# Optimization experiments

Hardware: AMD Instinct MI355X
Metric: run time of the kernel (lower is better)

The kernel has to match this reference:

```python
import jax, jax.numpy as jnp
import numpy as np

CAPACITY = 0.5


def setup_inputs() -> dict:
    key = jax.random.key(0)
    ks = jax.random.split(key, 5)
    B, L, D = 4, 4096, 1024
    Dff = 4 * D
    x = jax.random.normal(ks[0], (B, L, D), dtype=jnp.float32)
    w_router = jax.random.normal(ks[1], (D,), dtype=jnp.float32) / np.sqrt(D)
    w_bypass = jax.random.normal(ks[2], (D, D), dtype=jnp.float32) / np.sqrt(D)
    w1 = jax.random.normal(ks[3], (Dff, D), dtype=jnp.float32) / np.sqrt(D)
    w2 = jax.random.normal(ks[4], (D, Dff), dtype=jnp.float32) / np.sqrt(Dff)
    return {"x": x, "w_router": w_router, "w_bypass": w_bypass, "w1": w1, "w2": w2}


def _block_fn(x, w1, w2):
    # stand-in for the expensive full block: 2-layer GELU FFN (torch Linear: y = x W^T)
    h = jax.nn.gelu(jnp.einsum('bld,fd->blf', x, w1))
    return jnp.einsum('blf,df->bld', h, w2)


def reference(x, w_router, w_bypass, w1, w2):
    B, L, D = x.shape
    k = max(1, int(L * CAPACITY))  # static
    if k >= L:
        return _block_fn(x, w1, w2)
    # router scores (B, L)
    scores = jnp.einsum('bld,d->bl', x, w_router)
    _, top_idx = jax.lax.top_k(scores, k)          # (B, k)
    top_idx = jnp.sort(top_idx, axis=-1)           # (B, k), sorted positions
    # gather selected tokens -> (B, k, D)
    x_sel = jnp.take_along_axis(x, top_idx[:, :, None], axis=1)
    out_sel = _block_fn(x_sel, w1, w2)             # (B, k, D)
    # bypass path for all tokens
    output = jnp.einsum('bld,ed->ble', x, w_bypass)
    # scatter block outputs back onto selected positions
    b_idx = jnp.arange(B)[:, None]                 # (B, 1)
    output = output.at[b_idx, top_idx].set(out_sel)
    return output
```

## Files before the change

### kernel.cpp

```cpp
#include <hip/hip_runtime.h>
#include <stdint.h>
#include <math.h>


typedef __attribute__((ext_vector_type(8))) __bf16 bf16x8;
typedef __attribute__((ext_vector_type(4))) __bf16 bf16x4;
typedef __attribute__((ext_vector_type(4))) float f32x4;

__device__ __forceinline__ void async_cp16(const __bf16* g, __bf16* l) {
    __builtin_amdgcn_global_load_lds(
        (__attribute__((address_space(1))) void*)g,
        (__attribute__((address_space(3))) void*)l,
        16, 0, 0);
}

__device__ __forceinline__ float gelu_tanh(float x) {
    float x3 = x * x * x;
    float t = tanhf(0.7978845608028654f * (x + 0.044715f * x3));
    return 0.5f * x * (1.0f + t);
}

__global__ __launch_bounds__(256) void cvt_bf16(
    const float* __restrict__ in, __bf16* __restrict__ out, int n)
{
    int i = (blockIdx.x * blockDim.x + threadIdx.x) * 8;
    if (i >= n) return;
    float4 a = *(const float4*)(in + i);
    float4 b = *(const float4*)(in + i + 4);
    bf16x8 v;
    v[0] = (__bf16)a.x; v[1] = (__bf16)a.y; v[2] = (__bf16)a.z; v[3] = (__bf16)a.w;
    v[4] = (__bf16)b.x; v[5] = (__bf16)b.y; v[6] = (__bf16)b.z; v[7] = (__bf16)b.w;
    *(bf16x8*)(out + i) = v;
}

__global__ __launch_bounds__(256) void router_scores(
    const float* __restrict__ x, const float* __restrict__ wr,
    float* __restrict__ scores)
{
    int wid  = (blockIdx.x * blockDim.x + threadIdx.x) >> 6;
    int lane = threadIdx.x & 63;
    const float* row = x + (size_t)wid * 1024;
    double s = 0.0;
    #pragma unroll
    for (int it = 0; it < 4; ++it) {
        int base = it * 256 + lane * 4;
        float4 xv = *(const float4*)(row + base);
        float4 wv = *(const float4*)(wr + base);
        s += (double)xv.x * wv.x + (double)xv.y * wv.y
           + (double)xv.z * wv.z + (double)xv.w * wv.w;
    }
    #pragma unroll
    for (int off = 32; off > 0; off >>= 1) s += __shfl_down(s, off, 64);
    if (lane == 0) scores[wid] = (float)s;
}

__global__ __launch_bounds__(1024) void topk_build(
    const float* __restrict__ scores,
    int* __restrict__ sel_rows, int* __restrict__ byp_rows)
{
    const int L = 4096, K = 2048;
    __shared__ unsigned long long key[4096];
    __shared__ int flag[4096];
    __shared__ int tsum[1024];
    int b = blockIdx.x, t = threadIdx.x;

    for (int i = t; i < L; i += 1024) {
        unsigned u = __float_as_uint(scores[b * L + i]);
        u = (u & 0x80000000u) ? ~u : (u | 0x80000000u);
        key[i] = ((unsigned long long)u << 32) | (unsigned)(L - 1 - i);
    }
    __syncthreads();

    for (int kk = 2; kk <= L; kk <<= 1) {
        for (int j = kk >> 1; j > 0; j >>= 1) {
            for (int i = t; i < L; i += 1024) {
                int p = i ^ j;
                if (p > i) {
                    unsigned long long a = key[i], c = key[p];
                    bool sw = ((i & kk) == 0) ? (a < c) : (a > c);
                    if (sw) { key[i] = c; key[p] = a; }
                }
            }
            __syncthreads();
        }
    }

    for (int s = t; s < L; s += 1024) {
        int idx = (L - 1) - (int)(key[s] & 0xffffffffu);
        flag[idx] = (s < K) ? 1 : 0;
    }
    __syncthreads();

    int base = t * 4;
    int f0 = flag[base], f1 = flag[base+1], f2 = flag[base+2], f3 = flag[base+3];
    tsum[t] = f0 + f1 + f2 + f3;
    __syncthreads();
    for (int off = 1; off < 1024; off <<= 1) {
        int v = tsum[t];
        if (t >= off) v += tsum[t - off];
        __syncthreads();
        tsum[t] = v;
        __syncthreads();
    }
    int run = (t > 0) ? tsum[t - 1] : 0;
    int fl[4] = {f0, f1, f2, f3};
    #pragma unroll
    for (int j = 0; j < 4; ++j) {
        int idx = base + j;
        if (fl[j]) { sel_rows[b * K + run] = b * L + idx; run++; }
        else       { byp_rows[b * (L - K) + (idx - run)] = b * L + idx; }
    }
}

template <bool GATHER_A, bool SCATTER_OUT, bool GELU_ACT, typename OT>
__global__ __launch_bounds__(256) void gemm_async(
    const __bf16* __restrict__ A, const __bf16* __restrict__ W,
    OT* __restrict__ Out, const int* __restrict__ rows,
    int K, int lda, int ldo)
{
    constexpr int BM = 128, BK = 64;
    __shared__ __align__(16) __bf16 As[BM * BK];
    __shared__ __align__(16) __bf16 Bs[BM * BK];
    __shared__ int rs[BM];

    const int tid = threadIdx.x;
    const int m0 = blockIdx.y * BM, n0 = blockIdx.x * BM;
    if (tid < BM) rs[tid] = rows ? rows[m0 + tid] : (m0 + tid);
    __syncthreads();

    const int sub = tid >> 3;
    const int gc  = (tid & 7) ^ (sub & 7);
    const __bf16* aptr[4]; const __bf16* bptr[4];
    __bf16* adst[4]; __bf16* bdst[4];
    #pragma unroll
    for (int i = 0; i < 4; ++i) {
        int row = i * 32 + sub;
        int ar  = GATHER_A ? rs[row] : (m0 + row);
        aptr[i] = A + (size_t)ar * lda + gc * 8;
        bptr[i] = W + (size_t)(n0 + row) * K + gc * 8;
        adst[i] = As + (i * 256 + tid) * 8;
        bdst[i] = Bs + (i * 256 + tid) * 8;
    }

    f32x4 acc[4][4] = {};
    const int lane = tid & 63;
    const int wv = tid >> 6;
    const int wr = (wv >> 1) * 64, wc = (wv & 1) * 64;
    const int r = lane & 15, quad = lane >> 4;

    for (int k0 = 0; k0 < K; k0 += BK) {
        #pragma unroll
        for (int i = 0; i < 4; ++i) async_cp16(aptr[i] + k0, adst[i]);
        #pragma unroll
        for (int i = 0; i < 4; ++i) async_cp16(bptr[i] + k0, bdst[i]);
        __syncthreads();

        #pragma unroll
        for (int ks = 0; ks < 2; ++ks) {
            bf16x8 af[4], bfm[4];
            #pragma unroll
            for (int mi = 0; mi < 4; ++mi) {
                int row = wr + mi * 16 + r;
                int swz = (ks * 4 + quad) ^ (row & 7);
                af[mi] = *(const bf16x8*)(As + row * BK + swz * 8);
            }
            #pragma unroll
            for (int ni = 0; ni < 4; ++ni) {
                int row = wc + ni * 16 + r;
                int swz = (ks * 4 + quad) ^ (row & 7);
                bfm[ni] = *(const bf16x8*)(Bs + row * BK + swz * 8);
            }
            #pragma unroll
            for (int mi = 0; mi < 4; ++mi)
                #pragma unroll
                for (int ni = 0; ni < 4; ++ni)
                    acc[mi][ni] = __builtin_amdgcn_mfma_f32_16x16x32_bf16(
                        af[mi], bfm[ni], acc[mi][ni], 0, 0, 0);
        }
        __syncthreads();
    }

    #pragma unroll
    for (int mi = 0; mi < 4; ++mi) {
        #pragma unroll
        for (int reg = 0; reg < 4; ++reg) {
            int rowl = wr + mi * 16 + quad * 4 + reg;
            int orow = SCATTER_OUT ? rs[rowl] : (m0 + rowl);
            OT* op = Out + (size_t)orow * ldo + n0;
            #pragma unroll
            for (int ni = 0; ni < 4; ++ni) {
                float v = acc[mi][ni][reg];
                if (GELU_ACT) v = gelu_tanh(v);
                op[wc + ni * 16 + r] = (OT)v;
            }
        }
    }
}

template <typename AT, typename OT, bool GATHER_A, bool SCATTER_OUT, bool GELU_ACT>
__global__ __launch_bounds__(256) void gemm_bt(
    const AT* __restrict__ A, const float* __restrict__ W,
    OT* __restrict__ Out, const int* __restrict__ rows,
    int K, int lda, int ldo)
{
    constexpr int BM = 128, BK = 64, LDK = 72;
    __shared__ __align__(16) __bf16 As[BM * LDK];
    __shared__ __align__(16) __bf16 Bs[BM * LDK];
    __shared__ int rs[BM];

    const int tid = threadIdx.x;
    const int m0 = blockIdx.y * BM, n0 = blockIdx.x * BM;
    if (tid < BM) rs[tid] = rows ? rows[m0 + tid] : (m0 + tid);
    __syncthreads();

    constexpr bool A_F32 = (sizeof(AT) == 4);
    constexpr int A_PASS = A_F32 ? 8 : 4;
    const int a_rowg = A_F32 ? (tid >> 4) : (tid >> 3);
    const int a_col  = A_F32 ? (tid & 15) : (tid & 7);
    const AT* aptr[A_PASS];
    int a_lrow[A_PASS];
    #pragma unroll
    for (int it = 0; it < A_PASS; ++it) {
        int row = it * (A_F32 ? 16 : 32) + a_rowg;
        int ar = GATHER_A ? rs[row] : (m0 + row);
        aptr[it] = A + (size_t)ar * lda + a_col * (A_F32 ? 4 : 8);
        a_lrow[it] = row;
    }
    const int b_rowg = tid >> 4, b_col = tid & 15;
    const float* bptr[8];
    #pragma unroll
    for (int it = 0; it < 8; ++it)
        bptr[it] = W + (size_t)(n0 + it * 16 + b_rowg) * K + b_col * 4;

    f32x4 acc[4][4] = {};
    const int lane = tid & 63;
    const int wv = tid >> 6;
    const int wr = (wv >> 1) * 64, wc = (wv & 1) * 64;
    const int r = lane & 15, quad = lane >> 4;

    for (int k0 = 0; k0 < K; k0 += BK) {
        #pragma unroll
        for (int it = 0; it < A_PASS; ++it) {
            if (A_F32) {
                float4 v = *(const float4*)((const float*)aptr[it] + k0);
                bf16x4 w;
                w[0] = (__bf16)v.x; w[1] = (__bf16)v.y;
                w[2] = (__bf16)v.z; w[3] = (__bf16)v.w;
                *(bf16x4*)(As + a_lrow[it] * LDK + a_col * 4) = w;
            } else {
                bf16x8 v = *(const bf16x8*)((const __bf16*)aptr[it] + k0);
                *(bf16x8*)(As + a_lrow[it] * LDK + a_col * 8) = v;
            }
        }
        #pragma unroll
        for (int it = 0; it < 8; ++it) {
            float4 v = *(const float4*)(bptr[it] + k0);
            bf16x4 w;
            w[0] = (__bf16)v.x; w[1] = (__bf16)v.y;
            w[2] = (__bf16)v.z; w[3] = (__bf16)v.w;
            *(bf16x4*)(Bs + (it * 16 + b_rowg) * LDK + b_col * 4) = w;
        }
        __syncthreads();

        #pragma unroll
        for (int ks = 0; ks < 2; ++ks) {
            bf16x8 af[4], bfm[4];
            #pragma unroll
            for (int mi = 0; mi < 4; ++mi) {
                int row = wr + mi * 16 + r;
                af[mi] = *(const bf16x8*)(As + row * LDK + (ks * 4 + quad) * 8);
            }
            #pragma unroll
            for (int ni = 0; ni < 4; ++ni) {
                int row = wc + ni * 16 + r;
                bfm[ni] = *(const bf16x8*)(Bs + row * LDK + (ks * 4 + quad) * 8);
            }
            #pragma unroll
            for (int mi = 0; mi < 4; ++mi)
                #pragma unroll
                for (int ni = 0; ni < 4; ++ni)
                    acc[mi][ni] = __builtin_amdgcn_mfma_f32_16x16x32_bf16(
                        af[mi], bfm[ni], acc[mi][ni], 0, 0, 0);
        }
        __syncthreads();
    }

    #pragma unroll
    for (int mi = 0; mi < 4; ++mi) {
        #pragma unroll
        for (int reg = 0; reg < 4; ++reg) {
            int rowl = wr + mi * 16 + quad * 4 + reg;
            int orow = SCATTER_OUT ? rs[rowl] : (m0 + rowl);
            OT* op = Out + (size_t)orow * ldo + n0;
            #pragma unroll
            for (int ni = 0; ni < 4; ++ni) {
                float v = acc[mi][ni][reg];
                if (GELU_ACT) v = gelu_tanh(v);
                op[wc + ni * 16 + r] = (OT)v;
            }
        }
    }
}

extern "C" void kernel_launch(void* const* d_in, const int* in_sizes, int n_in,
                              void* d_out, int out_size, void* d_ws, size_t ws_size,
                              hipStream_t stream) {
    (void)in_sizes; (void)n_in; (void)out_size;
    const float* x  = (const float*)d_in[0];
    const float* wr = (const float*)d_in[1];
    const float* wb = (const float*)d_in[2];
    const float* w1 = (const float*)d_in[3];
    const float* w2 = (const float*)d_in[4];
    float* out = (float*)d_out;

    const int B = 4, L = 4096, D = 1024, DFF = 4096, KSEL = 2048;
    const int M = B * KSEL;
    const int NTOK = B * L;

    char* ws = (char*)d_ws;
    float* scores = (float*)ws;            ws += sizeof(float) * (size_t)NTOK;
    int* sel_rows = (int*)ws;              ws += sizeof(int) * (size_t)M;
    int* byp_rows = (int*)ws;              ws += sizeof(int) * (size_t)M;
    uintptr_t up = ((uintptr_t)ws + 255) & ~(uintptr_t)255;

    size_t n_x = (size_t)NTOK * D, n_wb = (size_t)D * D;
    size_t n_w1 = (size_t)DFF * D, n_w2 = (size_t)D * DFF;
    size_t n_h = (size_t)M * DFF;
    size_t needA = (up - (uintptr_t)d_ws)
                 + 2 * (n_x + n_wb + n_w1 + n_w2 + n_h) + 1024;

    router_scores<<<NTOK / 4, 256, 0, stream>>>(x, wr, scores);
    topk_build<<<B, 1024, 0, stream>>>(scores, sel_rows, byp_rows);

    if (ws_size >= needA) {
        __bf16* xb  = (__bf16*)up;        up += 2 * n_x;
        __bf16* wbb = (__bf16*)up;        up += 2 * n_wb;
        __bf16* w1b = (__bf16*)up;        up += 2 * n_w1;
        __bf16* w2b = (__bf16*)up;        up += 2 * n_w2;
        up = (up + 255) & ~(uintptr_t)255;
        __bf16* h   = (__bf16*)up;

        cvt_bf16<<<(int)(n_x  / 8 + 255) / 256 * 1 + ((n_x % 2048)?1:0), 256, 0, stream>>>(x,  xb,  (int)n_x);
        cvt_bf16<<<(int)((n_wb / 8 + 255) / 256), 256, 0, stream>>>(wb, wbb, (int)n_wb);
        cvt_bf16<<<(int)((n_w1 / 8 + 255) / 256), 256, 0, stream>>>(w1, w1b, (int)n_w1);
        cvt_bf16<<<(int)((n_w2 / 8 + 255) / 256), 256, 0, stream>>>(w2, w2b, (int)n_w2);

        gemm_async<true, true, false, float>
            <<<dim3(D / 128, M / 128), 256, 0, stream>>>(
            xb, wbb, out, byp_rows, D, D, D);
        gemm_async<true, false, true, __bf16>
            <<<dim3(DFF / 128, M / 128), 256, 0, stream>>>(
            xb, w1b, h, sel_rows, D, D, DFF);
        gemm_async<false, true, false, float>
            <<<dim3(D / 128, M / 128), 256, 0, stream>>>(
            h, w2b, out, sel_rows, DFF, DFF, D);
    } else {
        __bf16* h = (__bf16*)up;
        gemm_bt<float, float, true, true, false>
            <<<dim3(D / 128, M / 128), 256, 0, stream>>>(
            x, wb, out, byp_rows, D, D, D);
        for (int b = 0; b < B; ++b) {
            const int* selc = sel_rows + b * KSEL;
            gemm_bt<float, __bf16, true, false, true>
                <<<dim3(DFF / 128, KSEL / 128), 256, 0, stream>>>(
                x, w1, h, selc, D, D, DFF);
            gemm_bt<__bf16, float, false, true, false>
                <<<dim3(D / 128, KSEL / 128), 256, 0, stream>>>(
                h, w2, out, selc, DFF, DFF, D);
        }
    }
}
```

Measured before the change: 443.8 us.

## Fuse x conversion into router, merge weight casts, combine bypass and FFN2 GEMMs

Computes router scores and the bf16 copy of x in one pass over x, so x is read once instead of twice. The three weight conversions become a single launch. The bypass GEMM and the second FFN GEMM run as one launch using a z grid dimension, which balances work across CUs in a single wave. GELU now uses a sigmoid-based approximation via __expf instead of tanhf. The fallback path for a small workspace is removed, so the code now assumes the workspace is large enough.

Measured after the change: 421.6 us. 5.0% less time.

```diff
diff --git a/kernel.cpp b/kernel.cpp
--- a/kernel.cpp
+++ b/kernel.cpp
@@ -4,7 +4,6 @@
 
 
 typedef __attribute__((ext_vector_type(8))) __bf16 bf16x8;
-typedef __attribute__((ext_vector_type(4))) __bf16 bf16x4;
 typedef __attribute__((ext_vector_type(4))) float f32x4;
 
 __device__ __forceinline__ void async_cp16(const __bf16* g, __bf16* l) {
@@ -14,44 +13,59 @@
         16, 0, 0);
 }
 
-__device__ __forceinline__ float gelu_tanh(float x) {
-    float x3 = x * x * x;
-    float t = tanhf(0.7978845608028654f * (x + 0.044715f * x3));
-    return 0.5f * x * (1.0f + t);
-}
-
-__global__ __launch_bounds__(256) void cvt_bf16(
-    const float* __restrict__ in, __bf16* __restrict__ out, int n)
-{
-    int i = (blockIdx.x * blockDim.x + threadIdx.x) * 8;
-    if (i >= n) return;
-    float4 a = *(const float4*)(in + i);
-    float4 b = *(const float4*)(in + i + 4);
+__device__ __forceinline__ float gelu_fast(float x) {
+    float u = 1.5957691216057308f * x * (1.0f + 0.044715f * x * x);
+    return x / (1.0f + __expf(-u));
+}
+
+__global__ __launch_bounds__(256) void router_cvt(
+    const float* __restrict__ x, const float* __restrict__ wr,
+    float* __restrict__ scores, __bf16* __restrict__ xb)
+{
+    int wid  = (blockIdx.x * blockDim.x + threadIdx.x) >> 6;
+    int lane = threadIdx.x & 63;
+    const float* row = x + (size_t)wid * 1024;
+    __bf16* orow = xb + (size_t)wid * 1024;
+    double s = 0.0;
+    #pragma unroll
+    for (int it = 0; it < 2; ++it) {
+        int base = it * 512 + lane * 8;
+        float4 a  = *(const float4*)(row + base);
+        float4 b  = *(const float4*)(row + base + 4);
+        float4 wa = *(const float4*)(wr + base);
+        float4 wc = *(const float4*)(wr + base + 4);
+        s += (double)a.x * wa.x + (double)a.y * wa.y
+           + (double)a.z * wa.z + (double)a.w * wa.w
+           + (double)b.x * wc.x + (double)b.y * wc.y
+           + (double)b.z * wc.z + (double)b.w * wc.w;
+        bf16x8 v;
+        v[0] = (__bf16)a.x; v[1] = (__bf16)a.y; v[2] = (__bf16)a.z; v[3] = (__bf16)a.w;
+        v[4] = (__bf16)b.x; v[5] = (__bf16)b.y; v[6] = (__bf16)b.z; v[7] = (__bf16)b.w;
+        *(bf16x8*)(orow + base) = v;
+    }
+    #pragma unroll
+    for (int off = 32; off > 0; off >>= 1) s += __shfl_down(s, off, 64);
+    if (lane == 0) scores[wid] = (float)s;
+}
+
+__global__ __launch_bounds__(256) void cvt3(
+    const float* __restrict__ p0, const float* __restrict__ p1,
+    const float* __restrict__ p2,
+    __bf16* __restrict__ o0, __bf16* __restrict__ o1, __bf16* __restrict__ o2,
+    int c0, int c1, int c2)
+{
+    int chunk = blockIdx.x * 256 + threadIdx.x;
+    const float* in; __bf16* out;
+    if (chunk < c0)                { in = p0 + (size_t)chunk * 8;             out = o0 + (size_t)chunk * 8; }
+    else if (chunk < c0 + c1)      { int c = chunk - c0;      in = p1 + (size_t)c * 8; out = o1 + (size_t)c * 8; }
+    else if (chunk < c0 + c1 + c2) { int c = chunk - c0 - c1; in = p2 + (size_t)c * 8; out = o2 + (size_t)c * 8; }
+    else return;
+    float4 a = *(const float4*)(in);
+    float4 b = *(const float4*)(in + 4);
     bf16x8 v;
     v[0] = (__bf16)a.x; v[1] = (__bf16)a.y; v[2] = (__bf16)a.z; v[3] = (__bf16)a.w;
     v[4] = (__bf16)b.x; v[5] = (__bf16)b.y; v[6] = (__bf16)b.z; v[7] = (__bf16)b.w;
-    *(bf16x8*)(out + i) = v;
-}
-
-__global__ __launch_bounds__(256) void router_scores(
-    const float* __restrict__ x, const float* __restrict__ wr,
-    float* __restrict__ scores)
-{
-    int wid  = (blockIdx.x * blockDim.x + threadIdx.x) >> 6;
-    int lane = threadIdx.x & 63;
-    const float* row = x + (size_t)wid * 1024;
-    double s = 0.0;
-    #pragma unroll
-    for (int it = 0; it < 4; ++it) {
-        int base = it * 256 + lane * 4;
-        float4 xv = *(const float4*)(row + base);
-        float4 wv = *(const float4*)(wr + base);
-        s += (double)xv.x * wv.x + (double)xv.y * wv.y
-           + (double)xv.z * wv.z + (double)xv.w * wv.w;
-    }
-    #pragma unroll
-    for (int off = 32; off > 0; off >>= 1) s += __shfl_down(s, off, 64);
-    if (lane == 0) scores[wid] = (float)s;
+    *(bf16x8*)(out) = v;
 }
 
 __global__ __launch_bounds__(1024) void topk_build(
@@ -190,76 +204,61 @@
             #pragma unroll
             for (int ni = 0; ni < 4; ++ni) {
                 float v = acc[mi][ni][reg];
-                if (GELU_ACT) v = gelu_tanh(v);
+                if (GELU_ACT) v = gelu_fast(v);
                 op[wc + ni * 16 + r] = (OT)v;
             }
         }
     }
 }
 
-template <typename AT, typename OT, bool GATHER_A, bool SCATTER_OUT, bool GELU_ACT>
-__global__ __launch_bounds__(256) void gemm_bt(
-    const AT* __restrict__ A, const float* __restrict__ W,
-    OT* __restrict__ Out, const int* __restrict__ rows,
-    int K, int lda, int ldo)
-{
-    constexpr int BM = 128, BK = 64, LDK = 72;
-    __shared__ __align__(16) __bf16 As[BM * LDK];
-    __shared__ __align__(16) __bf16 Bs[BM * LDK];
+__global__ __launch_bounds__(256) void gemm_tail(
+    const __bf16* __restrict__ h, const __bf16* __restrict__ w2b,
+    const __bf16* __restrict__ xb, const __bf16* __restrict__ wbb,
+    float* __restrict__ Out,
+    const int* __restrict__ sel_rows, const int* __restrict__ byp_rows)
+{
+    constexpr int BM = 128, BK = 64;
+    __shared__ __align__(16) __bf16 As[BM * BK];
+    __shared__ __align__(16) __bf16 Bs[BM * BK];
     __shared__ int rs[BM];
+
+    const int z = blockIdx.z;
+    const __bf16* A = z ? xb : h;
+    const __bf16* W = z ? wbb : w2b;
+    const int K = z ? 1024 : 4096;
+    const int* rows = z ? byp_rows : sel_rows;
+    const bool gat = (z != 0);
 
     const int tid = threadIdx.x;
     const int m0 = blockIdx.y * BM, n0 = blockIdx.x * BM;
-    if (tid < BM) rs[tid] = rows ? rows[m0 + tid] : (m0 + tid);
-    __syncthreads();
-
-    constexpr bool A_F32 = (sizeof(AT) == 4);
-    constexpr int A_PASS = A_F32 ? 8 : 4;
-    const int a_rowg = A_F32 ? (tid >> 4) : (tid >> 3);
-    const int a_col  = A_F32 ? (tid & 15) : (tid & 7);
-    const AT* aptr[A_PASS];
-    int a_lrow[A_PASS];
-    #pragma unroll
-    for (int it = 0; it < A_PASS; ++it) {
-        int row = it * (A_F32 ? 16 : 32) + a_rowg;
-        int ar = GATHER_A ? rs[row] : (m0 + row);
-        aptr[it] = A + (size_t)ar * lda + a_col * (A_F32 ? 4 : 8);
-        a_lrow[it] = row;
-    }
-    const int b_rowg = tid >> 4, b_col = tid & 15;
-    const float* bptr[8];
-    #pragma unroll
-    for (int it = 0; it < 8; ++it)
-        bptr[it] = W + (size_t)(n0 + it * 16 + b_rowg) * K + b_col * 4;
+    rs[tid & 127] = rows[m0 + (tid & 127)];
+    __syncthreads();
+
+    const int sub = tid >> 3;
+    const int gc  = (tid & 7) ^ (sub & 7);
+    const __bf16* aptr[4]; const __bf16* bptr[4];
+    __bf16* adst[4]; __bf16* bdst[4];
+    #pragma unroll
+    for (int i = 0; i < 4; ++i) {
+        int row = i * 32 + sub;
+        int ar  = gat ? rs[row] : (m0 + row);
+        aptr[i] = A + (size_t)ar * K + gc * 8;
+        bptr[i] = W + (size_t)(n0 + row) * K + gc * 8;
+        adst[i] = As + (i * 256 + tid) * 8;
+        bdst[i] = Bs + (i * 256 + tid) * 8;
+    }
 
     f32x4 acc[4][4] = {};
     const int lane = tid & 63;
     const int wv = tid >> 6;
-    const int wr = (wv >> 1) * 64, wc = (wv & 1) * 64;
+    const int wrr = (wv >> 1) * 64, wc = (wv & 1) * 64;
     const int r = lane & 15, quad = lane >> 4;
 
     for (int k0 = 0; k0 < K; k0 += BK) {
         #pragma unroll
-        for (int it = 0; it < A_PASS; ++it) {
-            if (A_F32) {
-                float4 v = *(const float4*)((const float*)aptr[it] + k0);
-                bf16x4 w;
-                w[0] = (__bf16)v.x; w[1] = (__bf16)v.y;
-                w[2] = (__bf16)v.z; w[3] = (__bf16)v.w;
-                *(bf16x4*)(As + a_lrow[it] * LDK + a_col * 4) = w;
-            } else {
-                bf16x8 v = *(const bf16x8*)((const __bf16*)aptr[it] + k0);
-                *(bf16x8*)(As + a_lrow[it] * LDK + a_col * 8) = v;
-            }
-        }
-        #pragma unroll
-        for (int it = 0; it < 8; ++it) {
-            float4 v = *(const float4*)(bptr[it] + k0);
-            bf16x4 w;
-            w[0] = (__bf16)v.x; w[1] = (__bf16)v.y;
-            w[2] = (__bf16)v.z; w[3] = (__bf16)v.w;
-            *(bf16x4*)(Bs + (it * 16 + b_rowg) * LDK + b_col * 4) = w;
-        }
+        for (int i = 0; i < 4; ++i) async_cp16(aptr[i] + k0, adst[i]);
+        #pragma unroll
+        for (int i = 0; i < 4; ++i) async_cp16(bptr[i] + k0, bdst[i]);
         __syncthreads();
 
         #pragma unroll
@@ -267,13 +266,15 @@
             bf16x8 af[4], bfm[4];
             #pragma unroll
             for (int mi = 0; mi < 4; ++mi) {
-                int row = wr + mi * 16 + r;
-                af[mi] = *(const bf16x8*)(As + row * LDK + (ks * 4 + quad) * 8);
+                int row = wrr + mi * 16 + r;
+                int swz = (ks * 4 + quad) ^ (row & 7);
+                af[mi] = *(const bf16x8*)(As + row * BK + swz * 8);
             }
             #pragma unroll
             for (int ni = 0; ni < 4; ++ni) {
                 int row = wc + ni * 16 + r;
-                bfm[ni] = *(const bf16x8*)(Bs + row * LDK + (ks * 4 + quad) * 8);
+                int swz = (ks * 4 + quad) ^ (row & 7);
+                bfm[ni] = *(const bf16x8*)(Bs + row * BK + swz * 8);
             }
             #pragma unroll
             for (int mi = 0; mi < 4; ++mi)
@@ -289,15 +290,12 @@
     for (int mi = 0; mi < 4; ++mi) {
         #pragma unroll
         for (int reg = 0; reg < 4; ++reg) {
-            int rowl = wr + mi * 16 + quad * 4 + reg;
-            int orow = SCATTER_OUT ? rs[rowl] : (m0 + rowl);
-            OT* op = Out + (size_t)orow * ldo + n0;
-            #pragma unroll
-            for (int ni = 0; ni < 4; ++ni) {
-                float v = acc[mi][ni][reg];
-                if (GELU_ACT) v = gelu_tanh(v);
-                op[wc + ni * 16 + r] = (OT)v;
-            }
+            int rowl = wrr + mi * 16 + quad * 4 + reg;
+            int orow = rs[rowl];
+            float* op = Out + (size_t)orow * 1024 + n0;
+            #pragma unroll
+            for (int ni = 0; ni < 4; ++ni)
+                op[wc + ni * 16 + r] = acc[mi][ni][reg];
         }
     }
 }
@@ -305,7 +303,7 @@
 extern "C" void kernel_launch(void* const* d_in, const int* in_sizes, int n_in,
                               void* d_out, int out_size, void* d_ws, size_t ws_size,
                               hipStream_t stream) {
-    (void)in_sizes; (void)n_in; (void)out_size;
+    (void)in_sizes; (void)n_in; (void)out_size; (void)ws_size;
     const float* x  = (const float*)d_in[0];
     const float* wr = (const float*)d_in[1];
     const float* wb = (const float*)d_in[2];
@@ -317,56 +315,30 @@
     const int M = B * KSEL;
     const int NTOK = B * L;
 
+    size_t n_x = (size_t)NTOK * D, n_wb = (size_t)D * D;
+    size_t n_w1 = (size_t)DFF * D, n_w2 = (size_t)D * DFF;
+
     char* ws = (char*)d_ws;
     float* scores = (float*)ws;            ws += sizeof(float) * (size_t)NTOK;
     int* sel_rows = (int*)ws;              ws += sizeof(int) * (size_t)M;
     int* byp_rows = (int*)ws;              ws += sizeof(int) * (size_t)M;
     uintptr_t up = ((uintptr_t)ws + 255) & ~(uintptr_t)255;
-
-    size_t n_x = (size_t)NTOK * D, n_wb = (size_t)D * D;
-    size_t n_w1 = (size_t)DFF * D, n_w2 = (size_t)D * DFF;
-    size_t n_h = (size_t)M * DFF;
-    size_t needA = (up - (uintptr_t)d_ws)
-                 + 2 * (n_x + n_wb + n_w1 + n_w2 + n_h) + 1024;
-
-    router_scores<<<NTOK / 4, 256, 0, stream>>>(x, wr, scores);
+    __bf16* xb  = (__bf16*)up;             up += 2 * n_x;
+    __bf16* wbb = (__bf16*)up;             up += 2 * n_wb;
+    __bf16* w1b = (__bf16*)up;             up += 2 * n_w1;
+    __bf16* w2b = (__bf16*)up;             up += 2 * n_w2;
+    up = (up + 255) & ~(uintptr_t)255;
+    __bf16* h   = (__bf16*)up;
+
+    router_cvt<<<NTOK / 4, 256, 0, stream>>>(x, wr, scores, xb);
+    cvt3<<<(int)((n_wb + n_w1 + n_w2) / 8 / 256), 256, 0, stream>>>(
+        wb, w1, w2, wbb, w1b, w2b,
+        (int)(n_wb / 8), (int)(n_w1 / 8), (int)(n_w2 / 8));
     topk_build<<<B, 1024, 0, stream>>>(scores, sel_rows, byp_rows);
 
-    if (ws_size >= needA) {
-        __bf16* xb  = (__bf16*)up;        up += 2 * n_x;
-        __bf16* wbb = (__bf16*)up;        up += 2 * n_wb;
-        __bf16* w1b = (__bf16*)up;        up += 2 * n_w1;
-        __bf16* w2b = (__bf16*)up;        up += 2 * n_w2;
-        up = (up + 255) & ~(uintptr_t)255;
-        __bf16* h   = (__bf16*)up;
-
-        cvt_bf16<<<(int)(n_x  / 8 + 255) / 256 * 1 + ((n_x % 2048)?1:0), 256, 0, stream>>>(x,  xb,  (int)n_x);
-        cvt_bf16<<<(int)((n_wb / 8 + 255) / 256), 256, 0, stream>>>(wb, wbb, (int)n_wb);
-        cvt_bf16<<<(int)((n_w1 / 8 + 255) / 256), 256, 0, stream>>>(w1, w1b, (int)n_w1);
-        cvt_bf16<<<(int)((n_w2 / 8 + 255) / 256), 256, 0, stream>>>(w2, w2b, (int)n_w2);
-
-        gemm_async<true, true, false, float>
-            <<<dim3(D / 128, M / 128), 256, 0, stream>>>(
-            xb, wbb, out, byp_rows, D, D, D);
-        gemm_async<true, false, true, __bf16>
-            <<<dim3(DFF / 128, M / 128), 256, 0, stream>>>(
-            xb, w1b, h, sel_rows, D, D, DFF);
-        gemm_async<false, true, false, float>
-            <<<dim3(D / 128, M / 128), 256, 0, stream>>>(
-            h, w2b, out, sel_rows, DFF, DFF, D);
-    } else {
-        __bf16* h = (__bf16*)up;
-        gemm_bt<float, float, true, true, false>
-            <<<dim3(D / 128, M / 128), 256, 0, stream>>>(
-            x, wb, out, byp_rows, D, D, D);
-        for (int b = 0; b < B; ++b) {
-            const int* selc = sel_rows + b * KSEL;
-            gemm_bt<float, __bf16, true, false, true>
-                <<<dim3(DFF / 128, KSEL / 128), 256, 0, stream>>>(
-                x, w1, h, selc, D, D, DFF);
-            gemm_bt<__bf16, float, false, true, false>
-                <<<dim3(D / 128, KSEL / 128), 256, 0, stream>>>(
-                h, w2, out, selc, DFF, DFF, D);
-        }
-    }
-}
+    gemm_async<true, false, true, __bf16>
+        <<<dim3(DFF / 128, M / 128), 256, 0, stream>>>(
+        xb, w1b, h, sel_rows, D, D, DFF);
+    gemm_tail<<<dim3(D / 128, M / 128, 2), 256, 0, stream>>>(
+        h, w2b, xb, wbb, out, sel_rows, byp_rows);
+}
```
